# Kernel tuning notes

Hardware: AMD Instinct MI355X
Metric: run time of the kernel (lower is better)

The kernel has to match this reference:

```python
import jax, jax.numpy as jnp
import numpy as np


def setup_inputs() -> dict:
    key = jax.random.key(0)
    kq, kk, kv = jax.random.split(key, 3)
    B, H, S, D = 4, 16, 2048, 64
    q = jax.random.normal(kq, (B, H, S, D), dtype=jnp.float32)
    k = jax.random.normal(kk, (B, H, S, D), dtype=jnp.float32)
    v = jax.random.normal(kv, (B, H, S, D), dtype=jnp.float32)
    # causal mask: True = attend, broadcasts over batch/head dims
    mask = jnp.tril(jnp.ones((S, S), dtype=bool))
    return {"q": q, "k": k, "v": v, "mask": mask}


def reference(q, k, v, mask):
    # att[b,h,i,j] = q[b,h,i,:] . k[b,h,j,:] / sqrt(d_k)
    scale = 1.0 / jnp.sqrt(jnp.asarray(k.shape[-1], dtype=q.dtype))
    att = jnp.einsum('bhqd,bhkd->bhqk', q, k) * scale
    att = jnp.where(mask, att, -jnp.inf)  # additive -inf mask, equivalent to att + where(mask,0,-inf)
    att = jax.nn.softmax(att, axis=-1)
    return jnp.einsum('bhqk,bhkd->bhqd', att, v)
```

## Files before the change

### kernel.cpp

```cpp
#include <hip/hip_runtime.h>
#include <hip/hip_bf16.h>

typedef __attribute__((ext_vector_type(4)))  float f32x4;
typedef __attribute__((ext_vector_type(16))) float f32x16;
typedef __attribute__((ext_vector_type(8)))  short bf16x8;
typedef __attribute__((ext_vector_type(4)))  short bf16x4;

constexpr int SEQ = 2048;
constexpr int DH  = 64;
constexpr int BH  = 64;
constexpr int QB  = 256;
constexpr int KB  = 64;
constexpr int NQT = SEQ / QB;
constexpr int NST = SEQ / 64;

__device__ __forceinline__ short f2bf(float f) {
    union { float f; unsigned u; } x; x.f = f;
    unsigned r = x.u + 0x7fffu + ((x.u >> 16) & 1u);
    return (short)(r >> 16);
}

__device__ __forceinline__ unsigned cvtpk(float lo, float hi) {
    unsigned r;
    asm("v_cvt_pk_bf16_f32 %0, %1, %2" : "=v"(r) : "v"(lo), "v"(hi));
    return r;
}

__device__ __forceinline__ float exp2fast(float x) {
#if __has_builtin(__builtin_amdgcn_exp2f)
    return __builtin_amdgcn_exp2f(x);
#else
    float r;
    asm("v_exp_f32 %0, %1\n\ts_nop 0" : "=v"(r) : "v"(x));
    return r;
#endif
}

__device__ __forceinline__ void half_swap(unsigned a, unsigned b, unsigned &x, unsigned &y) {
#if __has_builtin(__builtin_amdgcn_permlane32_swap)
    auto rr = __builtin_amdgcn_permlane32_swap(a, b, false, false);
    x = rr[0]; y = rr[1];
#else
    unsigned as = (unsigned)__shfl_xor((int)a, 32);
    unsigned bs = (unsigned)__shfl_xor((int)b, 32);
    const bool lo = ((threadIdx.x & 63) < 32);
    x = lo ? a : bs;
    y = lo ? as : b;
#endif
}

__global__ __launch_bounds__(256) void prep_kernel(
    const float* __restrict__ Kg, const float* __restrict__ Vg,
    short* __restrict__ Kb, short* __restrict__ Vt)
{
    __shared__ short sT[64][66];
    const int bid = blockIdx.x;
    const int bh  = bid & (BH - 1);
    const int st  = bid >> 6;
    const int s0  = st * 64;
    const size_t base = (size_t)bh * SEQ * DH;
    const int tid = threadIdx.x;

    #pragma unroll
    for (int it = 0; it < 4; ++it) {
        const int i4 = it * 256 + tid;
        const int r  = i4 >> 4;
        const int c4 = (i4 & 15) << 2;
        const size_t gidx = base + (size_t)(s0 + r) * DH + c4;
        f32x4 kx = *(const f32x4*)(Kg + gidx);
        bf16x4 kb4;
        #pragma unroll
        for (int j = 0; j < 4; ++j) kb4[j] = f2bf(kx[j]);
        *(bf16x4*)(Kb + gidx) = kb4;
        f32x4 vx = *(const f32x4*)(Vg + gidx);
        #pragma unroll
        for (int j = 0; j < 4; ++j) sT[r][c4 + j] = f2bf(vx[j]);
    }
    __syncthreads();

    const int d   = tid >> 2;
    const int seg = (tid & 3) * 16;
    bf16x8 lo, hi;
    #pragma unroll
    for (int m = 0; m < 8; ++m) { lo[m] = sT[seg + m][d]; hi[m] = sT[seg + 8 + m][d]; }
    short* Vo = Vt + base + (size_t)d * SEQ + (s0 + seg);
    *(bf16x8*)Vo       = lo;
    *(bf16x8*)(Vo + 8) = hi;
}

__global__ __launch_bounds__(512) void fattn4_kernel(
    const float* __restrict__ Qg, const short* __restrict__ Kb,
    const short* __restrict__ Vt, float* __restrict__ Og)
{
    __shared__ short sK[2][KB * DH];
    __shared__ short sV[2][DH * KB];

    const int bid = blockIdx.x;
    const int g   = bid >> 6;
    const int bh  = bid & 63;
    const int qt  = (g < 4) ? (7 - g) : (g - 4);
    const int q0  = qt * QB;

    const int tid  = threadIdx.x;
    const int wid  = tid >> 6;
    const int lane = tid & 63;
    const int l31  = lane & 31;
    const int hi   = lane >> 5;

    const size_t base = (size_t)bh * SEQ * DH;
    const float* Qb = Qg + base;
    const short* Kp = Kb + base;
    const short* Vp = Vt + base;

    const int qw = q0 + wid * 32;
    const int qr = qw + l31;

    const int rr = wid * 8 + (lane >> 3);
    const int cs = (lane & 7) ^ (rr & 7);
    const short* kSrc = Kp + (size_t)rr * DH + cs * 8;
    const short* vSrc = Vp + (size_t)rr * SEQ + cs * 8;

    auto ISSUE = [&](int t, int buf) {
        const int kv0 = t * KB;
        __builtin_amdgcn_global_load_lds(
            (const unsigned int*)(kSrc + (size_t)kv0 * DH),
            (unsigned int*)&sK[buf][wid * 512], 16, 0, 0);
        __builtin_amdgcn_global_load_lds(
            (const unsigned int*)(vSrc + kv0),
            (unsigned int*)&sV[buf][wid * 512], 16, 0, 0);
    };

    constexpr float QSCALE = 0.125f * 1.44269504088896340736f;
    bf16x8 qf[4];
    #pragma unroll
    for (int dt = 0; dt < 4; ++dt) {
        const float* qp = Qb + (size_t)qr * DH + dt * 16 + hi * 8;
        f32x4 a = *(const f32x4*)qp;
        f32x4 b = *(const f32x4*)(qp + 4);
        bf16x8 f;
        #pragma unroll
        for (int j = 0; j < 4; ++j) { f[j] = f2bf(a[j] * QSCALE); f[j + 4] = f2bf(b[j] * QSCALE); }
        qf[dt] = f;
    }

    f32x16 o0, o1;
    #pragma unroll
    for (int r = 0; r < 16; ++r) { o0[r] = 0.f; o1[r] = 0.f; }
    float m_i = -1e30f, l_i = 0.f;

    const int ntile = qt * 4 + 4;
    ISSUE(0, 0);
    __syncthreads();

    for (int t = 0; t < ntile; ++t) {
        const int kv0 = t * KB;
        const int cur = t & 1;
        if (t + 1 < ntile) ISSUE(t + 1, cur ^ 1);

        if (kv0 <= qw + 31) {
            const short* cK = &sK[cur][0];
            const short* cV = &sV[cur][0];

            f32x16 st0, st1;
            #pragma unroll
            for (int r = 0; r < 16; ++r) { st0[r] = 0.f; st1[r] = 0.f; }
            #pragma unroll
            for (int dt = 0; dt < 4; ++dt) {
                const int ca = dt * 32 + hi * 16;
                bf16x8 k0 = *(const bf16x8*)((const char*)cK + l31 * 128 + (ca ^ ((l31 & 7) << 4)));
                bf16x8 k1 = *(const bf16x8*)((const char*)cK + (32 + l31) * 128 + (ca ^ ((l31 & 7) << 4)));
                st0 = __builtin_amdgcn_mfma_f32_32x32x16_bf16(k0, qf[dt], st0, 0, 0, 0);
                st1 = __builtin_amdgcn_mfma_f32_32x32x16_bf16(k1, qf[dt], st1, 0, 0, 0);
            }

            if (kv0 + KB - 1 > qw) {
                #pragma unroll
                for (int r = 0; r < 16; ++r) {
                    const int kr = (r & 3) + 8 * (r >> 2) + 4 * hi;
                    if (kv0 + kr > qr)      st0[r] = -1e30f;
                    if (kv0 + 32 + kr > qr) st1[r] = -1e30f;
                }
            }

            float pm = st0[0];
            #pragma unroll
            for (int r = 1; r < 16; ++r) pm = fmaxf(pm, st0[r]);
            #pragma unroll
            for (int r = 0; r < 16; ++r) pm = fmaxf(pm, st1[r]);
            pm = fmaxf(pm, __shfl_xor(pm, 32));

            constexpr float THR = 8.0f * 1.44269504088896340736f;
            if (!__all(pm - m_i <= THR)) {
                const float nm = fmaxf(m_i, pm);
                const float cf = exp2fast(m_i - nm);
                #pragma unroll
                for (int r = 0; r < 16; ++r) {
                    const int kr = (r & 3) + 8 * (r >> 2) + 4 * hi;
                    const float cfr = __shfl(cf, kr);
                    o0[r] *= cfr; o1[r] *= cfr;
                }
                l_i *= cf;
                m_i = nm;
            }

            float rs = 0.f;
            #pragma unroll
            for (int r = 0; r < 16; ++r) { st0[r] = exp2fast(st0[r] - m_i); rs += st0[r]; }
            #pragma unroll
            for (int r = 0; r < 16; ++r) { st1[r] = exp2fast(st1[r] - m_i); rs += st1[r]; }
            rs += __shfl_xor(rs, 32);
            l_i += rs;

            bf16x8 pf[4];
            {
                unsigned pk[8];
                #pragma unroll
                for (int i = 0; i < 8; ++i) pk[i] = cvtpk(st0[2 * i], st0[2 * i + 1]);
                #pragma unroll
                for (int c = 0; c < 2; ++c) {
                    unsigned x0, y0, x1, y1;
                    half_swap(pk[4 * c + 0], pk[4 * c + 2], x0, y0);
                    half_swap(pk[4 * c + 1], pk[4 * c + 3], x1, y1);
                    union { unsigned u[4]; bf16x8 v; } uu;
                    uu.u[0] = x0; uu.u[1] = x1; uu.u[2] = y0; uu.u[3] = y1;
                    pf[c] = uu.v;
                }
                #pragma unroll
                for (int i = 0; i < 8; ++i) pk[i] = cvtpk(st1[2 * i], st1[2 * i + 1]);
                #pragma unroll
                for (int c = 0; c < 2; ++c) {
                    unsigned x0, y0, x1, y1;
                    half_swap(pk[4 * c + 0], pk[4 * c + 2], x0, y0);
                    half_swap(pk[4 * c + 1], pk[4 * c + 3], x1, y1);
                    union { unsigned u[4]; bf16x8 v; } uu;
                    uu.u[0] = x0; uu.u[1] = x1; uu.u[2] = y0; uu.u[3] = y1;
                    pf[2 + c] = uu.v;
                }
            }

            #pragma unroll
            for (int ks = 0; ks < 4; ++ks) {
                const int cv = ks * 32 + hi * 16;
                bf16x8 v0 = *(const bf16x8*)((const char*)cV + l31 * 128 + (cv ^ ((l31 & 7) << 4)));
                o0 = __builtin_amdgcn_mfma_f32_32x32x16_bf16(pf[ks], v0, o0, 0, 0, 0);
                bf16x8 v1 = *(const bf16x8*)((const char*)cV + (32 + l31) * 128 + (cv ^ ((l31 & 7) << 4)));
                o1 = __builtin_amdgcn_mfma_f32_32x32x16_bf16(pf[ks], v1, o1, 0, 0, 0);
            }
        }

        __syncthreads();
    }

    float* Ob = Og + base;
    #pragma unroll
    for (int r = 0; r < 16; ++r) {
        const int kr  = (r & 3) + 8 * (r >> 2) + 4 * hi;
        const float ll = __shfl(l_i, kr);
        const float inv = 1.0f / ll;
        const int row = qw + kr;
        Ob[(size_t)row * DH + l31]      = o0[r] * inv;
        Ob[(size_t)row * DH + 32 + l31] = o1[r] * inv;
    }
}

extern "C" void kernel_launch(void* const* d_in, const int* in_sizes, int n_in,
                              void* d_out, int out_size, void* d_ws, size_t ws_size,
                              hipStream_t stream) {
    const float* q = (const float*)d_in[0];
    const float* k = (const float*)d_in[1];
    const float* v = (const float*)d_in[2];
    float* out = (float*)d_out;

    short* Kb = (short*)d_ws;
    short* Vt = Kb + (size_t)BH * SEQ * DH;

    prep_kernel<<<dim3(BH * NST), dim3(256), 0, stream>>>(k, v, Kb, Vt);
    fattn4_kernel<<<dim3(BH * NQT), dim3(512), 0, stream>>>(q, Kb, Vt, out);
}
```

Baseline: 80.63 us.

## Halve query tile to 128 rows with 4-wave blocks and interleaved causal scheduling

Reduces the query block from 256 to 128 rows and the block from 8 to 4 waves, with launch bounds asking for 4 blocks per CU. Block-to-tile mapping is reworked so heavy and light causal tiles interleave across the grid. Each wave now issues twice as many global-to-LDS loads, and the first K/V prefetch is moved ahead of the Q load. It also raises wave priority around the MFMA sections, uses tree reductions for the row max and split accumulators for the exp sum. The aim is better load balance and occupancy, at the cost of more blocks re-streaming K/V.

```diff
diff --git a/kernel.cpp b/kernel.cpp
--- a/kernel.cpp
+++ b/kernel.cpp
@@ -9,7 +9,7 @@
 constexpr int SEQ = 2048;
 constexpr int DH  = 64;
 constexpr int BH  = 64;
-constexpr int QB  = 256;
+constexpr int QB  = 128;
 constexpr int KB  = 64;
 constexpr int NQT = SEQ / QB;
 constexpr int NST = SEQ / 64;
@@ -88,7 +88,7 @@
     *(bf16x8*)(Vo + 8) = hi;
 }
 
-__global__ __launch_bounds__(512) void fattn4_kernel(
+__global__ __launch_bounds__(256, 4) void fattn5_kernel(
     const float* __restrict__ Qg, const short* __restrict__ Kb,
     const short* __restrict__ Vt, float* __restrict__ Og)
 {
@@ -96,9 +96,12 @@
     __shared__ short sV[2][DH * KB];
 
     const int bid = blockIdx.x;
-    const int g   = bid >> 6;
-    const int bh  = bid & 63;
-    const int qt  = (g < 4) ? (7 - g) : (g - 4);
+    const int c   = bid & 255;
+    const int grp = bid >> 8;
+    const int bh  = c >> 2;
+    const int a   = c & 3;
+    const int qt  = (grp == 0) ? (15 - a) : (grp == 1) ? (8 + a)
+                  : (grp == 2) ? (7 - a)  : a;
     const int q0  = qt * QB;
 
     const int tid  = threadIdx.x;
@@ -115,31 +118,35 @@
     const int qw = q0 + wid * 32;
     const int qr = qw + l31;
 
-    const int rr = wid * 8 + (lane >> 3);
-    const int cs = (lane & 7) ^ (rr & 7);
-    const short* kSrc = Kp + (size_t)rr * DH + cs * 8;
-    const short* vSrc = Vp + (size_t)rr * SEQ + cs * 8;
+    const int rrow = wid * 16 + (lane >> 3);
+    const int cs   = (lane & 7) ^ (rrow & 7);
+    const short* kSrc = Kp + (size_t)rrow * DH + cs * 8;
+    const short* vSrc = Vp + (size_t)rrow * SEQ + cs * 8;
 
     auto ISSUE = [&](int t, int buf) {
         const int kv0 = t * KB;
-        __builtin_amdgcn_global_load_lds(
-            (const unsigned int*)(kSrc + (size_t)kv0 * DH),
-            (unsigned int*)&sK[buf][wid * 512], 16, 0, 0);
-        __builtin_amdgcn_global_load_lds(
-            (const unsigned int*)(vSrc + kv0),
-            (unsigned int*)&sV[buf][wid * 512], 16, 0, 0);
+        __builtin_amdgcn_global_load_lds((const unsigned int*)(kSrc + (size_t)kv0 * DH),
+                                         (unsigned int*)&sK[buf][wid * 1024], 16, 0, 0);
+        __builtin_amdgcn_global_load_lds((const unsigned int*)(kSrc + (size_t)kv0 * DH + 8 * DH),
+                                         (unsigned int*)&sK[buf][wid * 1024 + 512], 16, 0, 0);
+        __builtin_amdgcn_global_load_lds((const unsigned int*)(vSrc + kv0),
+                                         (unsigned int*)&sV[buf][wid * 1024], 16, 0, 0);
+        __builtin_amdgcn_global_load_lds((const unsigned int*)(vSrc + kv0 + 8 * SEQ),
+                                         (unsigned int*)&sV[buf][wid * 1024 + 512], 16, 0, 0);
     };
+
+    ISSUE(0, 0);
 
     constexpr float QSCALE = 0.125f * 1.44269504088896340736f;
     bf16x8 qf[4];
     #pragma unroll
     for (int dt = 0; dt < 4; ++dt) {
         const float* qp = Qb + (size_t)qr * DH + dt * 16 + hi * 8;
-        f32x4 a = *(const f32x4*)qp;
-        f32x4 b = *(const f32x4*)(qp + 4);
+        f32x4 av = *(const f32x4*)qp;
+        f32x4 bv = *(const f32x4*)(qp + 4);
         bf16x8 f;
         #pragma unroll
-        for (int j = 0; j < 4; ++j) { f[j] = f2bf(a[j] * QSCALE); f[j + 4] = f2bf(b[j] * QSCALE); }
+        for (int j = 0; j < 4; ++j) { f[j] = f2bf(av[j] * QSCALE); f[j + 4] = f2bf(bv[j] * QSCALE); }
         qf[dt] = f;
     }
 
@@ -148,8 +155,7 @@
     for (int r = 0; r < 16; ++r) { o0[r] = 0.f; o1[r] = 0.f; }
     float m_i = -1e30f, l_i = 0.f;
 
-    const int ntile = qt * 4 + 4;
-    ISSUE(0, 0);
+    const int ntile = 2 * qt + 2;
     __syncthreads();
 
     for (int t = 0; t < ntile; ++t) {
@@ -164,6 +170,7 @@
             f32x16 st0, st1;
             #pragma unroll
             for (int r = 0; r < 16; ++r) { st0[r] = 0.f; st1[r] = 0.f; }
+            __builtin_amdgcn_s_setprio(1);
             #pragma unroll
             for (int dt = 0; dt < 4; ++dt) {
                 const int ca = dt * 32 + hi * 16;
@@ -172,6 +179,7 @@
                 st0 = __builtin_amdgcn_mfma_f32_32x32x16_bf16(k0, qf[dt], st0, 0, 0, 0);
                 st1 = __builtin_amdgcn_mfma_f32_32x32x16_bf16(k1, qf[dt], st1, 0, 0, 0);
             }
+            __builtin_amdgcn_s_setprio(0);
 
             if (kv0 + KB - 1 > qw) {
                 #pragma unroll
@@ -182,12 +190,15 @@
                 }
             }
 
-            float pm = st0[0];
-            #pragma unroll
-            for (int r = 1; r < 16; ++r) pm = fmaxf(pm, st0[r]);
-            #pragma unroll
-            for (int r = 0; r < 16; ++r) pm = fmaxf(pm, st1[r]);
-            pm = fmaxf(pm, __shfl_xor(pm, 32));
+            float mx[8];
+            #pragma unroll
+            for (int r = 0; r < 8; ++r)
+                mx[r] = fmaxf(fmaxf(st0[r], st0[r + 8]), fmaxf(st1[r], st1[r + 8]));
+            #pragma unroll
+            for (int s = 4; s > 0; s >>= 1)
+                #pragma unroll
+                for (int r = 0; r < s; ++r) mx[r] = fmaxf(mx[r], mx[r + s]);
+            float pm = fmaxf(mx[0], __shfl_xor(mx[0], 32));
 
             constexpr float THR = 8.0f * 1.44269504088896340736f;
             if (!__all(pm - m_i <= THR)) {
@@ -203,11 +214,22 @@
                 m_i = nm;
             }
 
-            float rs = 0.f;
-            #pragma unroll
-            for (int r = 0; r < 16; ++r) { st0[r] = exp2fast(st0[r] - m_i); rs += st0[r]; }
-            #pragma unroll
-            for (int r = 0; r < 16; ++r) { st1[r] = exp2fast(st1[r] - m_i); rs += st1[r]; }
+            float rs0 = 0.f, rs1 = 0.f, rs2 = 0.f, rs3 = 0.f;
+            #pragma unroll
+            for (int r = 0; r < 16; r += 4) {
+                st0[r]     = exp2fast(st0[r]     - m_i); rs0 += st0[r];
+                st0[r + 1] = exp2fast(st0[r + 1] - m_i); rs1 += st0[r + 1];
+                st0[r + 2] = exp2fast(st0[r + 2] - m_i); rs2 += st0[r + 2];
+                st0[r + 3] = exp2fast(st0[r + 3] - m_i); rs3 += st0[r + 3];
+            }
+            #pragma unroll
+            for (int r = 0; r < 16; r += 4) {
+                st1[r]     = exp2fast(st1[r]     - m_i); rs0 += st1[r];
+                st1[r + 1] = exp2fast(st1[r + 1] - m_i); rs1 += st1[r + 1];
+                st1[r + 2] = exp2fast(st1[r + 2] - m_i); rs2 += st1[r + 2];
+                st1[r + 3] = exp2fast(st1[r + 3] - m_i); rs3 += st1[r + 3];
+            }
+            float rs = (rs0 + rs1) + (rs2 + rs3);
             rs += __shfl_xor(rs, 32);
             l_i += rs;
 
@@ -217,27 +239,28 @@
                 #pragma unroll
                 for (int i = 0; i < 8; ++i) pk[i] = cvtpk(st0[2 * i], st0[2 * i + 1]);
                 #pragma unroll
-                for (int c = 0; c < 2; ++c) {
+                for (int cc = 0; cc < 2; ++cc) {
                     unsigned x0, y0, x1, y1;
-                    half_swap(pk[4 * c + 0], pk[4 * c + 2], x0, y0);
-                    half_swap(pk[4 * c + 1], pk[4 * c + 3], x1, y1);
+                    half_swap(pk[4 * cc + 0], pk[4 * cc + 2], x0, y0);
+                    half_swap(pk[4 * cc + 1], pk[4 * cc + 3], x1, y1);
                     union { unsigned u[4]; bf16x8 v; } uu;
                     uu.u[0] = x0; uu.u[1] = x1; uu.u[2] = y0; uu.u[3] = y1;
-                    pf[c] = uu.v;
+                    pf[cc] = uu.v;
                 }
                 #pragma unroll
                 for (int i = 0; i < 8; ++i) pk[i] = cvtpk(st1[2 * i], st1[2 * i + 1]);
                 #pragma unroll
-                for (int c = 0; c < 2; ++c) {
+                for (int cc = 0; cc < 2; ++cc) {
                     unsigned x0, y0, x1, y1;
-                    half_swap(pk[4 * c + 0], pk[4 * c + 2], x0, y0);
-                    half_swap(pk[4 * c + 1], pk[4 * c + 3], x1, y1);
+                    half_swap(pk[4 * cc + 0], pk[4 * cc + 2], x0, y0);
+                    half_swap(pk[4 * cc + 1], pk[4 * cc + 3], x1, y1);
                     union { unsigned u[4]; bf16x8 v; } uu;
                     uu.u[0] = x0; uu.u[1] = x1; uu.u[2] = y0; uu.u[3] = y1;
-                    pf[2 + c] = uu.v;
+                    pf[2 + cc] = uu.v;
                 }
             }
 
+            __builtin_amdgcn_s_setprio(1);
             #pragma unroll
             for (int ks = 0; ks < 4; ++ks) {
                 const int cv = ks * 32 + hi * 16;
@@ -246,6 +269,7 @@
                 bf16x8 v1 = *(const bf16x8*)((const char*)cV + (32 + l31) * 128 + (cv ^ ((l31 & 7) << 4)));
                 o1 = __builtin_amdgcn_mfma_f32_32x32x16_bf16(pf[ks], v1, o1, 0, 0, 0);
             }
+            __builtin_amdgcn_s_setprio(0);
         }
 
         __syncthreads();
@@ -275,5 +299,5 @@
     short* Vt = Kb + (size_t)BH * SEQ * DH;
 
     prep_kernel<<<dim3(BH * NST), dim3(256), 0, stream>>>(k, v, Kb, Vt);
-    fattn4_kernel<<<dim3(BH * NQT), dim3(512), 0, stream>>>(q, Kb, Vt, out);
-}
+    fattn5_kernel<<<dim3(BH * NQT), dim3(256), 0, stream>>>(q, Kb, Vt, out);
+}
```

Result: no change. 79.61 us (-1.3%).
